# Kernel optimization log

Hardware: AMD Instinct MI355X
Metric: run time of the kernel (lower is better)

Reference implementation:

```python
import jax, jax.numpy as jnp
import numpy as np
from jax import lax

# Static config (matches init_kwargs / electrode montage)
B, T, V = 16, 1536, 64
F1, D, H = 16, 2, 4
F2 = F1 * D              # 32
FO = F2 // H             # 8, GAT per-head out dim
K1, K3 = 32, 16          # conv kernel sizes (temporal)
P1, P2 = 8, 4            # avg pool sizes
KNN = 4
EPS = 1e-5
NEG_SLOPE = 0.2          # PyG GATConv leaky_relu slope


def _build_edges():
    # deterministic electrode geometry -> kNN graph, plus PyG self-loops
    rng = np.random.RandomState(0)
    pos = rng.randn(V, 3)
    dmat = np.linalg.norm(pos[:, None] - pos[None, :], axis=-1)
    order = np.argsort(dmat, axis=1)
    nbrs = order[:, 1:KNN + 1]                      # exclude self
    src = np.repeat(np.arange(V), KNN)
    dst = nbrs.reshape(-1)
    # add self loops (GATConv default add_self_loops=True)
    src = np.concatenate([src, np.arange(V)])
    dst = np.concatenate([dst, np.arange(V)])
    return jnp.asarray(np.stack([src, dst]), dtype=jnp.int32)  # (2, E)


def _bn(x, g, b, m, v, axis):
    shp = [1] * x.ndim
    shp[axis] = -1
    rs = lambda a: a.reshape(shp)
    return rs(g) * (x - rs(m)) * lax.rsqrt(rs(v) + EPS) + rs(b)


def _conv_same_t(x, w, k):
    # Conv2d(..., (1,k), padding='same'): torch pads (k-1)//2 left, rest right
    lp = (k - 1) // 2
    return lax.conv_general_dilated(x, w, (1, 1), [(0, 0), (lp, k - 1 - lp)],
                                    dimension_numbers=('NCHW', 'OIHW', 'NCHW'))


def _gat(x, W, a_src, a_dst, bias, src, dst):
    # Batched PyG GATConv (eval mode, dropout off), concat heads.
    # x: (Ng, V, F1); W: (F1, H*FO); a_src/a_dst: (H, FO); bias: (H*FO,)
    Ng = x.shape[0]
    h = jnp.einsum('nvf,fho->nvho', x, W.reshape(F1, H, FO))   # (Ng,V,H,FO)
    es = jnp.einsum('nvho,ho->nvh', h, a_src)[:, src]          # (Ng,E,H)
    ed = jnp.einsum('nvho,ho->nvh', h, a_dst)[:, dst]
    e = jax.nn.leaky_relu(es + ed, NEG_SLOPE)
    # softmax over incoming edges of each target node (segment softmax)
    m = jnp.full((Ng, V, H), -1e30, e.dtype).at[:, dst].max(e)
    ex = jnp.exp(e - m[:, dst])
    den = jnp.zeros((Ng, V, H), e.dtype).at[:, dst].add(ex)
    alpha = ex / den[:, dst]                                   # (Ng,E,H)
    out = jnp.zeros((Ng, V, H, FO), e.dtype).at[:, dst].add(alpha[..., None] * h[:, src])
    return out.reshape(Ng, V, H * FO) + bias


def setup_inputs() -> dict:
    key = jax.random.key(0)
    ks = jax.random.split(key, 16)
    bn = lambda k, c: (1.0 + 0.1 * jax.random.normal(jax.random.fold_in(k, 0), (c,)),
                       0.1 * jax.random.normal(jax.random.fold_in(k, 1), (c,)),
                       0.1 * jax.random.normal(jax.random.fold_in(k, 2), (c,)),
                       0.5 + jax.random.uniform(jax.random.fold_in(k, 3), (c,)))
    bn1 = bn(ks[1], F1); bn2 = bn(ks[2], F2); bn3 = bn(ks[3], F2)
    inp = {
        'x': jax.random.normal(ks[0], (B, 1, V, T), jnp.float32),
        'conv1_w': 0.1 * jax.random.normal(ks[4], (F1, 1, 1, K1), jnp.float32),
        'bn1_g': bn1[0], 'bn1_b': bn1[1], 'bn1_m': bn1[2], 'bn1_v': bn1[3],
        'gat_w': (1.0 / np.sqrt(F1)) * jax.random.normal(ks[5], (F1, H * FO), jnp.float32),
        'gat_asrc': 0.3 * jax.random.normal(ks[6], (H, FO), jnp.float32),
        'gat_adst': 0.3 * jax.random.normal(ks[7], (H, FO), jnp.float32),
        'gat_bias': 0.05 * jax.random.normal(ks[8], (H * FO,), jnp.float32),
        'bn2_g': bn2[0], 'bn2_b': bn2[1], 'bn2_m': bn2[2], 'bn2_v': bn2[3],
        'conv3_w': 0.1 * jax.random.normal(ks[9], (F2, F2, 1, K3), jnp.float32),
        'bn3_g': bn3[0], 'bn3_b': bn3[1], 'bn3_m': bn3[2], 'bn3_v': bn3[3],
        'edge_index': _build_edges(),
    }
    return inp


def reference(x, conv1_w, bn1_g, bn1_b, bn1_m, bn1_v,
              gat_w, gat_asrc, gat_adst, gat_bias,
              bn2_g, bn2_b, bn2_m, bn2_v,
              conv3_w, bn3_g, bn3_b, bn3_m, bn3_v, edge_index):
    src, dst = edge_index[0], edge_index[1]
    # block1: temporal conv + BN
    h = _conv_same_t(x, conv1_w, K1)                 # (B,F1,V,T)
    h = _bn(h, bn1_g, bn1_b, bn1_m, bn1_v, 1)
    # spatial GNN over B*T independent electrode graphs
    xg = h.transpose(0, 3, 2, 1).reshape(B * T, V, F1)
    g = _gat(xg, gat_w, gat_asrc, gat_adst, gat_bias, src, dst)   # (BT,V,F2)
    g = g.mean(axis=1).reshape(B, T, F2).transpose(0, 2, 1)       # (B,F2,T)
    g = _bn(g, bn2_g, bn2_b, bn2_m, bn2_v, 1)[:, :, None, :]      # (B,F2,1,T)
    # tail: elu -> pool -> conv -> bn -> elu -> pool (dropout = eval no-op)
    h = jax.nn.elu(g)
    h = h.reshape(B, F2, 1, T // P1, P1).mean(-1)
    h = _conv_same_t(h, conv3_w, K3)
    h = _bn(h, bn3_g, bn3_b, bn3_m, bn3_v, 1)
    h = jax.nn.elu(h)
    h = h.reshape(B, F2, 1, T // P1 // P2, P2).mean(-1)           # (B,F2,1,48)
    return h
```

## Files before the change

### kernel.cpp

```cpp
#include <hip/hip_runtime.h>
#include <math.h>

#define TPB 256

constexpr int Bc = 16, Tc = 1536;
constexpr int T2c = 192;
constexpr float EPSc = 1e-5f;
constexpr float NSLOPE = 0.2f;
constexpr int MDI = 16;
constexpr int MDO = 8;
constexpr float L2E = 1.4426950408889634f;

typedef float vf2 __attribute__((ext_vector_type(2)));

constexpr int OW_WEFF = 0;
constexpr int OW_CHL  = 1024;
constexpr int OW_CES  = 1056;
constexpr int OW_WSD  = 1064;
constexpr int OW_A2C2 = 1320;
constexpr int OW_WFT  = 1384;
constexpr int OW_GRAPH= 2408;
constexpr int OW_P    = 2825;


constexpr int L_XT  = 0;
constexpr int L_WB  = 2720;
constexpr int L_Y   = 4896;
constexpr int L_TOT = 6208;

#define LGKM0() __asm__ volatile("s_waitcnt lgkmcnt(0)" ::: "memory")

__device__ __forceinline__ int xt_idx(int row, int g, int lo)
{
    return L_XT + row * 68 + (((g + row) & 15) << 2) + lo;
}

__device__ __forceinline__ float lexp2(float z)
{
    return __builtin_amdgcn_exp2f(fmaxf(z, NSLOPE * z));
}

__device__ __forceinline__ float bfly16_sum(float s)
{
#if __has_builtin(__builtin_amdgcn_permlane16_swap)
    unsigned u = __builtin_bit_cast(unsigned, s);
    auto r = __builtin_amdgcn_permlane16_swap(u, u, false, false);
    return __builtin_bit_cast(float, (unsigned)r[0]) +
           __builtin_bit_cast(float, (unsigned)r[1]);
#else
    return s + __shfl_xor(s, 16);
#endif
}

__device__ __forceinline__ float bfly32_sum(float s)
{
#if __has_builtin(__builtin_amdgcn_permlane32_swap)
    unsigned u = __builtin_bit_cast(unsigned, s);
    auto r = __builtin_amdgcn_permlane32_swap(u, u, false, false);
    return __builtin_bit_cast(float, (unsigned)r[0]) +
           __builtin_bit_cast(float, (unsigned)r[1]);
#else
    return s + __shfl_xor(s, 32);
#endif
}

__global__ void prep_kernel(const float* __restrict__ c1w,
                            const float* __restrict__ g1, const float* __restrict__ b1,
                            const float* __restrict__ m1, const float* __restrict__ v1,
                            const float* __restrict__ W,
                            const float* __restrict__ asrc, const float* __restrict__ adst,
                            const float* __restrict__ bias,
                            const float* __restrict__ g2, const float* __restrict__ b2,
                            const float* __restrict__ m2, const float* __restrict__ v2,
                            const int* __restrict__ ei, int ne, float* __restrict__ ws)
{
    const int tid = threadIdx.x;
    __shared__ float sweff[1024];
    __shared__ float schl[32];
    __shared__ int isrcp_i[64 * MDI];
    __shared__ int outdst_i[64 * MDO];
    __shared__ int inslot[64], outslot[64];

    for (int idx = tid; idx < 1024; idx += TPB) {
        int k = idx >> 5, f2 = idx & 31;
        float s = 0.f;
        for (int f = 0; f < 16; f++) {
            float a1 = g1[f] * rsqrtf(v1[f] + EPSc);
            s += a1 * W[f * 32 + f2] * c1w[f * 32 + k];
        }
        ws[OW_WEFF + idx] = s;
        ws[OW_WFT + f2 * 32 + k] = s;
        sweff[idx] = s;
    }
    for (int f2 = tid; f2 < 32; f2 += TPB) {
        float s = 0.f;
        for (int f = 0; f < 16; f++) {
            float a1 = g1[f] * rsqrtf(v1[f] + EPSc);
            s = fmaf(b1[f] - a1 * m1[f], W[f * 32 + f2], s);
        }
        ws[OW_CHL + f2] = s;
        schl[f2] = s;
        float a2 = g2[f2] * rsqrtf(v2[f2] + EPSc);
        ws[OW_A2C2 + f2] = a2;
        ws[OW_A2C2 + 32 + f2] = b2[f2] + a2 * (bias[f2] - m2[f2] + s);
    }

    for (int i = tid; i < 64 * MDI; i += TPB) isrcp_i[i] = 0;
    for (int i = tid; i < 64 * MDO; i += TPB) outdst_i[i] = 0;
    if (tid < 64) { inslot[tid] = 0; outslot[tid] = 0; }
    __syncthreads();
    for (int e = tid; e < ne; e += TPB) {
        int s = ei[e], d = ei[ne + e];
        if (s == d) continue;
        int pi = atomicAdd(&inslot[d], 1);
        if (pi < 15) isrcp_i[d * MDI + pi] = s;
        int po = atomicAdd(&outslot[s], 1);
        if (po < MDO) outdst_i[s * MDO + po] = d;
    }
    __syncthreads();

    if (tid < 128) {
        int k = tid >> 2, h = tid & 3;
        float s1 = 0.f, s2 = 0.f;
        for (int o = 0; o < 8; o++) {
            float wv = sweff[k * 32 + h * 8 + o];
            s1 = fmaf(asrc[h * 8 + o], wv, s1);
            s2 = fmaf(adst[h * 8 + o], wv, s2);
        }
        ws[OW_WSD + h * 64 + k * 2]     = s1;
        ws[OW_WSD + h * 64 + k * 2 + 1] = s2;
    }
    if (tid < 4) {
        float s1 = 0.f, s2 = 0.f;
        for (int o = 0; o < 8; o++) {
            float cv = schl[tid * 8 + o];
            s1 = fmaf(asrc[tid * 8 + o], cv, s1);
            s2 = fmaf(adst[tid * 8 + o], cv, s2);
        }
        ws[OW_CES + tid * 2]     = s1;
        ws[OW_CES + tid * 2 + 1] = s2;
    }
    unsigned char* gb = (unsigned char*)(ws + OW_GRAPH);
    for (int i = tid; i < 64 * MDI; i += TPB) gb[i] = (unsigned char)isrcp_i[i];
    for (int i = tid; i < 64 * MDO; i += TPB) gb[1088 + i] = (unsigned char)outdst_i[i];
    __syncthreads();
    if (tid < 64) {
        int id = inslot[tid] < 15 ? inslot[tid] : 15;
        int od = outslot[tid] < MDO ? outslot[tid] : MDO;
        gb[tid * MDI + 15] = (unsigned char)id;
        gb[1024 + tid] = (unsigned char)id;
        gb[1600 + tid] = (unsigned char)od;
    }
    __syncthreads();
    if (tid == 0) {
        int mi = 0;
        for (int d = 0; d < 64; d++) {
            int a = gb[1024 + d];
            mi = a > mi ? a : mi;
        }
        gb[1664] = (unsigned char)mi;
        gb[1665] = 0;
    }
}

__global__ __launch_bounds__(TPB, 4) void gat_kernel(
    const float* __restrict__ x,
    const float* __restrict__ wfTp,
    const float* __restrict__ cesg,
    const float* __restrict__ wsdg,
    const float* __restrict__ a2c2,
    const int* __restrict__ graphi,
    float* __restrict__ pout)
{
    __shared__ __align__(16) float sm[L_TOT];

    const int tid  = threadIdx.x;
    const int b    = blockIdx.x / 192;
    const int tile = blockIdx.x % 192;
    const int t0   = tile * 8;

    const int h = tid >> 6, v = tid & 63;

    const unsigned char* gbg = (const unsigned char*)graphi;
    const int4 il = *(const int4*)(gbg + v * MDI);
    const unsigned ow = *(const unsigned*)(gbg + 1088 + v * MDO);
    const int mdin = __builtin_amdgcn_readfirstlane(((const int*)graphi)[416] & 0xFF);

    for (int idx = tid; idx < 2560; idx += TPB) {
        const int vv = idx / 40, j = idx % 40;
        float val = 1.0f;
        if (j < 39) {
            const int t = t0 - 15 + j;
            val = (t >= 0 && t < Tc) ? x[(b * 64 + vv) * Tc + t] : 0.f;
        }
        sm[xt_idx(j, vv >> 2, vv & 3)] = val;
    }
    __syncthreads();

    const int hs = __builtin_amdgcn_readfirstlane(h);
    const vf2* wsdh = (const vf2*)(wsdg + hs * 64);

    float aes[8], aed[8];
    {
        const int g = v >> 2, lo = v & 3;
        const vf2 cv = *(const vf2*)(cesg + hs * 2);
        vf2 acc2[8];
        #pragma unroll
        for (int t = 0; t < 8; t++) acc2[t] = cv;
        float xr[8];
        #pragma unroll
        for (int q = 0; q < 7; q++) xr[q] = sm[xt_idx(q, g, lo)];
        #pragma unroll
        for (int k = 0; k < 32; k++) {
            xr[(k + 7) & 7] = sm[xt_idx(k + 7, g, lo)];
            const vf2 wk = wsdh[k];
            #pragma unroll
            for (int t = 0; t < 8; t++) {
                const float xv = xr[(k + t) & 7];
                acc2[t] += (vf2){xv, xv} * wk;
            }
        }
        #pragma unroll
        for (int t = 0; t < 8; t++) {
            aes[t] = acc2[t].x * L2E;
            aed[t] = acc2[t].y * L2E;
        }
    }

    {
        float* esL0 = &sm[L_Y + h * 328];
        float* esL1 = &sm[L_WB + h * 544];

        const int indeg = (int)(((unsigned)il.w) >> 24);
        const unsigned iw[4] = {(unsigned)il.x, (unsigned)il.y,
                                (unsigned)il.z, (unsigned)il.w};

        float den[8], Eself[8];
        #pragma unroll
        for (int t = 0; t < 8; t++) {
            Eself[t] = lexp2(aes[t] + aed[t]);
            den[t] = Eself[t];
        }

        *(float4*)(esL0 + v * 4) = (float4){aes[0], aes[1], aes[2], aes[3]};
        *(float4*)(esL1 + v * 4) = (float4){aes[4], aes[5], aes[6], aes[7]};
        LGKM0();
        #pragma unroll
        for (int e = 0; e < 15; e++) {
            if (e < mdin) {
                const int s = (int)((iw[e >> 2] >> ((e & 3) * 8)) & 0xFF);
                const float4 ea = *(const float4*)(esL0 + s * 4);
                const float4 eb = *(const float4*)(esL1 + s * 4);
                const float valid = (e < indeg) ? 1.f : 0.f;
                den[0] += valid * lexp2(ea.x + aed[0]);
                den[1] += valid * lexp2(ea.y + aed[1]);
                den[2] += valid * lexp2(ea.z + aed[2]);
                den[3] += valid * lexp2(ea.w + aed[3]);
                den[4] += valid * lexp2(eb.x + aed[4]);
                den[5] += valid * lexp2(eb.y + aed[5]);
                den[6] += valid * lexp2(eb.z + aed[6]);
                den[7] += valid * lexp2(eb.w + aed[7]);
            }
        }
        LGKM0();

        float rden[8], wb[8];
        #pragma unroll
        for (int t = 0; t < 8; t++) {
            float r = __builtin_amdgcn_rcpf(den[t]);
            r = r * (2.f - den[t] * r);
            rden[t] = r;
            wb[t] = Eself[t] * r;
        }

        #pragma unroll
        for (int hf = 0; hf < 2; hf++) {
            const int tb4 = hf * 4;
            *(float4*)(esL0 + v * 4) = (float4){aed[tb4 + 0], aed[tb4 + 1],
                                                rden[tb4 + 0], rden[tb4 + 1]};
            *(float4*)(esL1 + v * 4) = (float4){aed[tb4 + 2], aed[tb4 + 3],
                                                rden[tb4 + 2], rden[tb4 + 3]};
            LGKM0();
            #pragma unroll
            for (int j = 0; j < 4; j++) {
                const int d = (int)((ow >> (j * 8)) & 0xFF);
                const float4 g0 = *(const float4*)(esL0 + d * 4);
                const float4 g1 = *(const float4*)(esL1 + d * 4);
                wb[tb4 + 0] = fmaf(lexp2(aes[tb4 + 0] + g0.x), g0.z, wb[tb4 + 0]);
                wb[tb4 + 1] = fmaf(lexp2(aes[tb4 + 1] + g0.y), g0.w, wb[tb4 + 1]);
                wb[tb4 + 2] = fmaf(lexp2(aes[tb4 + 2] + g1.x), g1.z, wb[tb4 + 2]);
                wb[tb4 + 3] = fmaf(lexp2(aes[tb4 + 3] + g1.y), g1.w, wb[tb4 + 3]);
            }
            LGKM0();
        }

        #pragma unroll
        for (int t = 0; t < 8; t++)
            sm[L_WB + h * 544 + t * 68 + v] = wb[t];
    }
    LGKM0();

    {
        const int cg = v & 7;
        const int th = (v >> 3) & 1;
        const int kq = v >> 4;

        vf2 yp[4][5];
        #pragma unroll
        for (int i = 0; i < 4; i++)
            #pragma unroll
            for (int q = 0; q < 5; q++) yp[i][q] = (vf2){0.f, 0.f};

        const float* wbbase = &sm[L_WB + h * 544 + (th * 4) * 68];
        #pragma unroll
        for (int v4 = 0; v4 < 4; v4++) {
            const int vcol = kq * 16 + v4 * 4;
            float4 wrow[4];
            #pragma unroll
            for (int i = 0; i < 4; i++)
                wrow[i] = *(const float4*)(wbbase + i * 68 + vcol);
            #pragma unroll
            for (int q = 0; q < 5; q++) {
                const int row = cg * 5 + q;
                const int mg = ((kq * 4 + v4 + row) & 15) << 2;
                const float4 x4 = *(const float4*)(&sm[L_XT + row * 68 + mg]);
                const vf2 x01 = (vf2){x4.x, x4.y}, x23 = (vf2){x4.z, x4.w};
                #pragma unroll
                for (int i = 0; i < 4; i++) {
                    const vf2 w01 = (vf2){wrow[i].x, wrow[i].y};
                    const vf2 w23 = (vf2){wrow[i].z, wrow[i].w};
                    yp[i][q] += w01 * x01;
                    yp[i][q] += w23 * x23;
                }
            }
        }
        float ya[4][5];
        #pragma unroll
        for (int i = 0; i < 4; i++)
            #pragma unroll
            for (int q = 0; q < 5; q++) {
                float s = yp[i][q].x + yp[i][q].y;
                ya[i][q] = bfly32_sum(bfly16_sum(s));
            }
        float* yw = &sm[L_Y + h * 328 + (th * 4 + kq) * 41 + cg * 5];
        #pragma unroll
        for (int q = 0; q < 5; q++) {
            float a01 = (kq & 1) ? ya[1][q] : ya[0][q];
            float a23 = (kq & 1) ? ya[3][q] : ya[2][q];
            yw[q] = (kq & 2) ? a23 : a01;
        }
    }
    LGKM0();

    {
        const int t = v >> 3, o = v & 7;
        const int f2d = h * 8 + o;
        const float4* wf4 = (const float4*)(wfTp + f2d * 32);

        const float* yr = &sm[L_Y + h * 328 + t * 41];
        float acc = 0.f;
        #pragma unroll
        for (int k4 = 0; k4 < 8; k4++) {
            const float4 w = wf4[k4];
            acc = fmaf(w.x, yr[t + 4 * k4 + 0],
                  fmaf(w.y, yr[t + 4 * k4 + 1],
                  fmaf(w.z, yr[t + 4 * k4 + 2],
                  fmaf(w.w, yr[t + 4 * k4 + 3], acc))));
        }

        const float a2 = a2c2[f2d], c2 = a2c2[32 + f2d];
        float y = fmaf(a2, acc * (1.f / 64.f), c2);
        y = y > 0.f ? y : __expf(y) - 1.f;
        y += __shfl_xor(y, 8);
        y = bfly32_sum(bfly16_sum(y));
        if (v < 8)
            pout[(b * T2c + tile) * 32 + h * 8 + v] = y * 0.125f;
    }
}

__global__ __launch_bounds__(TPB) void conv3_kernel(const float* __restrict__ pp,
                                                    const float* __restrict__ w3,
                                                    const float* __restrict__ g3,
                                                    const float* __restrict__ b3,
                                                    const float* __restrict__ m3,
                                                    const float* __restrict__ v3,
                                                    float* __restrict__ outp)
{
    __shared__ float pl[63 * 32];
    __shared__ float q[48 * 32];
    const int tid = threadIdx.x;
    const int b = blockIdx.x >> 2, cc = blockIdx.x & 3;

    for (int idx = tid; idx < 63 * 32; idx += TPB) {
        int r = idx >> 5, f2 = idx & 31;
        int tog = cc * 48 - 7 + r;
        pl[idx] = (tog >= 0 && tog < T2c) ? pp[(b * T2c + tog) * 32 + f2] : 0.f;
    }
    __syncthreads();

    const int f2o = tid & 31, grp = tid >> 5;
    const int tb = grp * 6;
    float acc[6] = { 0.f, 0.f, 0.f, 0.f, 0.f, 0.f };
    for (int f2i = 0; f2i < 32; f2i++) {
        float seg[21];
        #pragma unroll
        for (int r = 0; r < 21; r++) seg[r] = pl[(tb + r) * 32 + f2i];
        const float4* wrow = (const float4*)(w3 + (f2o * 32 + f2i) * 16);
        #pragma unroll
        for (int k4 = 0; k4 < 4; k4++) {
            const float4 w4 = wrow[k4];
            #pragma unroll
            for (int j = 0; j < 6; j++) {
                acc[j] = fmaf(seg[j + k4 * 4 + 0], w4.x,
                         fmaf(seg[j + k4 * 4 + 1], w4.y,
                         fmaf(seg[j + k4 * 4 + 2], w4.z,
                         fmaf(seg[j + k4 * 4 + 3], w4.w, acc[j]))));
            }
        }
    }
    const float a3 = g3[f2o] * rsqrtf(v3[f2o] + EPSc);
    const float c3 = b3[f2o] - a3 * m3[f2o];
    #pragma unroll
    for (int j = 0; j < 6; j++) {
        float y = fmaf(a3, acc[j], c3);
        y = y > 0.f ? y : __expf(y) - 1.f;
        q[(tb + j) * 32 + f2o] = y;
    }
    __syncthreads();
    for (int idx = tid; idx < 12 * 32; idx += TPB) {
        int t4 = idx >> 5, f2 = idx & 31;
        int r0 = t4 * 4;
        float s = q[r0 * 32 + f2] + q[(r0 + 1) * 32 + f2] +
                  q[(r0 + 2) * 32 + f2] + q[(r0 + 3) * 32 + f2];
        outp[(b * 32 + f2) * 48 + cc * 12 + t4] = s * 0.25f;
    }
}

extern "C" void kernel_launch(void* const* d_in, const int* in_sizes, int n_in,
                              void* d_out, int out_size, void* d_ws, size_t ws_size,
                              hipStream_t stream)
{
    const float* x    = (const float*)d_in[0];
    const float* c1w  = (const float*)d_in[1];
    const float* g1   = (const float*)d_in[2];
    const float* b1   = (const float*)d_in[3];
    const float* m1   = (const float*)d_in[4];
    const float* v1   = (const float*)d_in[5];
    const float* W    = (const float*)d_in[6];
    const float* asrc = (const float*)d_in[7];
    const float* adst = (const float*)d_in[8];
    const float* bias = (const float*)d_in[9];
    const float* g2   = (const float*)d_in[10];
    const float* b2   = (const float*)d_in[11];
    const float* m2   = (const float*)d_in[12];
    const float* v2   = (const float*)d_in[13];
    const float* w3   = (const float*)d_in[14];
    const float* g3   = (const float*)d_in[15];
    const float* b3   = (const float*)d_in[16];
    const float* m3   = (const float*)d_in[17];
    const float* v3   = (const float*)d_in[18];
    const int*   ei   = (const int*)d_in[19];
    const int    ne   = in_sizes[19] / 2;

    float* ws = (float*)d_ws;

    prep_kernel<<<1, TPB, 0, stream>>>(c1w, g1, b1, m1, v1, W, asrc, adst,
                                       bias, g2, b2, m2, v2, ei, ne, ws);

    gat_kernel<<<Bc * T2c, TPB, 0, stream>>>(x,
                                             ws + OW_WFT,
                                             ws + OW_CES,
                                             ws + OW_WSD,
                                             ws + OW_A2C2,
                                             (const int*)(ws + OW_GRAPH),
                                             ws + OW_P);

    conv3_kernel<<<Bc * 4, TPB, 0, stream>>>(ws + OW_P, w3, g3, b3, m3, v3,
                                             (float*)d_out);
}
```

Measured before the change: 161.2 us.

## Split GAT block work across 512 threads, two waves per head

The GAT kernel now launches 512 threads per block, and each head is served by two waves that each take half of the 8 timesteps. Per-thread register arrays shrink from 8 to 4 timesteps, and each wave pair gets its own scratch region in shared memory. Wave-local LGKM waits become block-wide barriers because the stages now share data across waves. The last projection stage runs only on half the waves. The aim is more parallelism and latency hiding per block, at the cost of extra __syncthreads and idle waves in the final stage.

```diff
diff --git a/kernel.cpp b/kernel.cpp
--- a/kernel.cpp
+++ b/kernel.cpp
@@ -2,6 +2,7 @@
 #include <math.h>
 
 #define TPB 256
+#define GTPB 512
 
 constexpr int Bc = 16, Tc = 1536;
 constexpr int T2c = 192;
@@ -163,7 +164,7 @@
     }
 }
 
-__global__ __launch_bounds__(TPB, 4) void gat_kernel(
+__global__ __launch_bounds__(GTPB, 8) void gat_kernel(
     const float* __restrict__ x,
     const float* __restrict__ wfTp,
     const float* __restrict__ cesg,
@@ -179,14 +180,17 @@
     const int tile = blockIdx.x % 192;
     const int t0   = tile * 8;
 
-    const int h = tid >> 6, v = tid & 63;
+    const int wid = tid >> 6;
+    const int h   = wid >> 1;
+    const int th  = wid & 1;
+    const int v   = tid & 63;
 
     const unsigned char* gbg = (const unsigned char*)graphi;
     const int4 il = *(const int4*)(gbg + v * MDI);
     const unsigned ow = *(const unsigned*)(gbg + 1088 + v * MDO);
     const int mdin = __builtin_amdgcn_readfirstlane(((const int*)graphi)[416] & 0xFF);
 
-    for (int idx = tid; idx < 2560; idx += TPB) {
+    for (int idx = tid; idx < 2560; idx += GTPB) {
         const int vv = idx / 40, j = idx % 40;
         float val = 1.0f;
         if (j < 39) {
@@ -197,162 +201,147 @@
     }
     __syncthreads();
 
-    const int hs = __builtin_amdgcn_readfirstlane(h);
+    const int hs  = __builtin_amdgcn_readfirstlane(h);
+    const int ths = __builtin_amdgcn_readfirstlane(th);
     const vf2* wsdh = (const vf2*)(wsdg + hs * 64);
 
-    float aes[8], aed[8];
+    float aes[4], aed[4];
     {
         const int g = v >> 2, lo = v & 3;
+        const int rb = ths * 4;
         const vf2 cv = *(const vf2*)(cesg + hs * 2);
-        vf2 acc2[8];
-        #pragma unroll
-        for (int t = 0; t < 8; t++) acc2[t] = cv;
-        float xr[8];
-        #pragma unroll
-        for (int q = 0; q < 7; q++) xr[q] = sm[xt_idx(q, g, lo)];
+        vf2 acc2[4];
+        #pragma unroll
+        for (int i = 0; i < 4; i++) acc2[i] = cv;
+        float xr[4];
+        #pragma unroll
+        for (int q = 0; q < 3; q++) xr[q] = sm[xt_idx(rb + q, g, lo)];
         #pragma unroll
         for (int k = 0; k < 32; k++) {
-            xr[(k + 7) & 7] = sm[xt_idx(k + 7, g, lo)];
+            xr[(k + 3) & 3] = sm[xt_idx(rb + k + 3, g, lo)];
             const vf2 wk = wsdh[k];
             #pragma unroll
-            for (int t = 0; t < 8; t++) {
-                const float xv = xr[(k + t) & 7];
-                acc2[t] += (vf2){xv, xv} * wk;
-            }
-        }
-        #pragma unroll
-        for (int t = 0; t < 8; t++) {
-            aes[t] = acc2[t].x * L2E;
-            aed[t] = acc2[t].y * L2E;
-        }
-    }
-
+            for (int i = 0; i < 4; i++) {
+                const float xv = xr[(k + i) & 3];
+                acc2[i] += (vf2){xv, xv} * wk;
+            }
+        }
+        #pragma unroll
+        for (int i = 0; i < 4; i++) {
+            aes[i] = acc2[i].x * L2E;
+            aed[i] = acc2[i].y * L2E;
+        }
+    }
+
+    float wb[4];
     {
-        float* esL0 = &sm[L_Y + h * 328];
-        float* esL1 = &sm[L_WB + h * 544];
+        float* scr = &sm[L_WB + h * 544 + th * 272];
 
         const int indeg = (int)(((unsigned)il.w) >> 24);
         const unsigned iw[4] = {(unsigned)il.x, (unsigned)il.y,
                                 (unsigned)il.z, (unsigned)il.w};
 
-        float den[8], Eself[8];
-        #pragma unroll
-        for (int t = 0; t < 8; t++) {
-            Eself[t] = lexp2(aes[t] + aed[t]);
-            den[t] = Eself[t];
-        }
-
-        *(float4*)(esL0 + v * 4) = (float4){aes[0], aes[1], aes[2], aes[3]};
-        *(float4*)(esL1 + v * 4) = (float4){aes[4], aes[5], aes[6], aes[7]};
+        float den[4], Eself[4];
+        #pragma unroll
+        for (int i = 0; i < 4; i++) {
+            Eself[i] = lexp2(aes[i] + aed[i]);
+            den[i] = Eself[i];
+        }
+
+        *(float4*)(scr + v * 4) = (float4){aes[0], aes[1], aes[2], aes[3]};
         LGKM0();
         #pragma unroll
         for (int e = 0; e < 15; e++) {
             if (e < mdin) {
                 const int s = (int)((iw[e >> 2] >> ((e & 3) * 8)) & 0xFF);
-                const float4 ea = *(const float4*)(esL0 + s * 4);
-                const float4 eb = *(const float4*)(esL1 + s * 4);
+                const float4 ea = *(const float4*)(scr + s * 4);
                 const float valid = (e < indeg) ? 1.f : 0.f;
                 den[0] += valid * lexp2(ea.x + aed[0]);
                 den[1] += valid * lexp2(ea.y + aed[1]);
                 den[2] += valid * lexp2(ea.z + aed[2]);
                 den[3] += valid * lexp2(ea.w + aed[3]);
-                den[4] += valid * lexp2(eb.x + aed[4]);
-                den[5] += valid * lexp2(eb.y + aed[5]);
-                den[6] += valid * lexp2(eb.z + aed[6]);
-                den[7] += valid * lexp2(eb.w + aed[7]);
             }
         }
         LGKM0();
 
-        float rden[8], wb[8];
-        #pragma unroll
-        for (int t = 0; t < 8; t++) {
-            float r = __builtin_amdgcn_rcpf(den[t]);
-            r = r * (2.f - den[t] * r);
-            rden[t] = r;
-            wb[t] = Eself[t] * r;
-        }
-
-        #pragma unroll
-        for (int hf = 0; hf < 2; hf++) {
-            const int tb4 = hf * 4;
-            *(float4*)(esL0 + v * 4) = (float4){aed[tb4 + 0], aed[tb4 + 1],
-                                                rden[tb4 + 0], rden[tb4 + 1]};
-            *(float4*)(esL1 + v * 4) = (float4){aed[tb4 + 2], aed[tb4 + 3],
-                                                rden[tb4 + 2], rden[tb4 + 3]};
+        float rden[4];
+        #pragma unroll
+        for (int i = 0; i < 4; i++) {
+            float r = __builtin_amdgcn_rcpf(den[i]);
+            r = r * (2.f - den[i] * r);
+            rden[i] = r;
+            wb[i] = Eself[i] * r;
+        }
+
+        #pragma unroll
+        for (int r2 = 0; r2 < 2; r2++) {
+            const int tb = r2 * 2;
+            *(float4*)(scr + v * 4) = (float4){aed[tb], aed[tb + 1],
+                                               rden[tb], rden[tb + 1]};
             LGKM0();
             #pragma unroll
             for (int j = 0; j < 4; j++) {
                 const int d = (int)((ow >> (j * 8)) & 0xFF);
-                const float4 g0 = *(const float4*)(esL0 + d * 4);
-                const float4 g1 = *(const float4*)(esL1 + d * 4);
-                wb[tb4 + 0] = fmaf(lexp2(aes[tb4 + 0] + g0.x), g0.z, wb[tb4 + 0]);
-                wb[tb4 + 1] = fmaf(lexp2(aes[tb4 + 1] + g0.y), g0.w, wb[tb4 + 1]);
-                wb[tb4 + 2] = fmaf(lexp2(aes[tb4 + 2] + g1.x), g1.z, wb[tb4 + 2]);
-                wb[tb4 + 3] = fmaf(lexp2(aes[tb4 + 3] + g1.y), g1.w, wb[tb4 + 3]);
+                const float4 g0 = *(const float4*)(scr + d * 4);
+                wb[tb + 0] = fmaf(lexp2(aes[tb + 0] + g0.x), g0.z, wb[tb + 0]);
+                wb[tb + 1] = fmaf(lexp2(aes[tb + 1] + g0.y), g0.w, wb[tb + 1]);
             }
             LGKM0();
         }
 
         #pragma unroll
-        for (int t = 0; t < 8; t++)
-            sm[L_WB + h * 544 + t * 68 + v] = wb[t];
-    }
-    LGKM0();
+        for (int i = 0; i < 4; i++)
+            sm[L_WB + h * 544 + (th * 4 + i) * 68 + v] = wb[i];
+    }
+    __syncthreads();
 
     {
         const int cg = v & 7;
-        const int th = (v >> 3) & 1;
+        const int tq = (v >> 3) & 1;
         const int kq = v >> 4;
 
-        vf2 yp[4][5];
-        #pragma unroll
-        for (int i = 0; i < 4; i++)
+        vf2 yp[2][5];
+        #pragma unroll
+        for (int i = 0; i < 2; i++)
             #pragma unroll
             for (int q = 0; q < 5; q++) yp[i][q] = (vf2){0.f, 0.f};
 
-        const float* wbbase = &sm[L_WB + h * 544 + (th * 4) * 68];
+        const float* wbb = &sm[L_WB + h * 544 + (th * 4 + tq * 2) * 68];
         #pragma unroll
         for (int v4 = 0; v4 < 4; v4++) {
             const int vcol = kq * 16 + v4 * 4;
-            float4 wrow[4];
-            #pragma unroll
-            for (int i = 0; i < 4; i++)
-                wrow[i] = *(const float4*)(wbbase + i * 68 + vcol);
+            const float4 w0 = *(const float4*)(wbb + vcol);
+            const float4 w1 = *(const float4*)(wbb + 68 + vcol);
             #pragma unroll
             for (int q = 0; q < 5; q++) {
                 const int row = cg * 5 + q;
                 const int mg = ((kq * 4 + v4 + row) & 15) << 2;
                 const float4 x4 = *(const float4*)(&sm[L_XT + row * 68 + mg]);
                 const vf2 x01 = (vf2){x4.x, x4.y}, x23 = (vf2){x4.z, x4.w};
-                #pragma unroll
-                for (int i = 0; i < 4; i++) {
-                    const vf2 w01 = (vf2){wrow[i].x, wrow[i].y};
-                    const vf2 w23 = (vf2){wrow[i].z, wrow[i].w};
-                    yp[i][q] += w01 * x01;
-                    yp[i][q] += w23 * x23;
-                }
-            }
-        }
-        float ya[4][5];
-        #pragma unroll
-        for (int i = 0; i < 4; i++)
+                yp[0][q] += (vf2){w0.x, w0.y} * x01;
+                yp[0][q] += (vf2){w0.z, w0.w} * x23;
+                yp[1][q] += (vf2){w1.x, w1.y} * x01;
+                yp[1][q] += (vf2){w1.z, w1.w} * x23;
+            }
+        }
+        float ya[2][5];
+        #pragma unroll
+        for (int i = 0; i < 2; i++)
             #pragma unroll
             for (int q = 0; q < 5; q++) {
                 float s = yp[i][q].x + yp[i][q].y;
                 ya[i][q] = bfly32_sum(bfly16_sum(s));
             }
-        float* yw = &sm[L_Y + h * 328 + (th * 4 + kq) * 41 + cg * 5];
-        #pragma unroll
-        for (int q = 0; q < 5; q++) {
-            float a01 = (kq & 1) ? ya[1][q] : ya[0][q];
-            float a23 = (kq & 1) ? ya[3][q] : ya[2][q];
-            yw[q] = (kq & 2) ? a23 : a01;
-        }
-    }
-    LGKM0();
-
-    {
+        if (kq < 2) {
+            float* yw = &sm[L_Y + h * 328 + (th * 4 + tq * 2 + kq) * 41 + cg * 5];
+            #pragma unroll
+            for (int q = 0; q < 5; q++)
+                yw[q] = (kq & 1) ? ya[1][q] : ya[0][q];
+        }
+    }
+    __syncthreads();
+
+    if (th == 0) {
         const int t = v >> 3, o = v & 7;
         const int f2d = h * 8 + o;
         const float4* wf4 = (const float4*)(wfTp + f2d * 32);
@@ -467,13 +456,13 @@
     prep_kernel<<<1, TPB, 0, stream>>>(c1w, g1, b1, m1, v1, W, asrc, adst,
                                        bias, g2, b2, m2, v2, ei, ne, ws);
 
-    gat_kernel<<<Bc * T2c, TPB, 0, stream>>>(x,
-                                             ws + OW_WFT,
-                                             ws + OW_CES,
-                                             ws + OW_WSD,
-                                             ws + OW_A2C2,
-                                             (const int*)(ws + OW_GRAPH),
-                                             ws + OW_P);
+    gat_kernel<<<Bc * T2c, GTPB, 0, stream>>>(x,
+                                              ws + OW_WFT,
+                                              ws + OW_CES,
+                                              ws + OW_WSD,
+                                              ws + OW_A2C2,
+                                              (const int*)(ws + OW_GRAPH),
+                                              ws + OW_P);
 
     conv3_kernel<<<Bc * 4, TPB, 0, stream>>>(ws + OW_P, w3, g3, b3, m3, v3,
                                              (float*)d_out);
```

Result: no change. 163.1 us (+1.2%).
